# Optimization experiments

Measured on AMD Instinct MI355X. Metric: run time of the kernel, lower is better.

Reference implementation:

```python
import jax, jax.numpy as jnp
import numpy as np

EPS = 1e-5


def hetero_layernorm(x, node_type, gamma, beta):
    # LayerNorm over feature dim with per-node-type affine params.
    mu = jnp.mean(x, axis=-1, keepdims=True)
    var = jnp.mean(jnp.square(x - mu), axis=-1, keepdims=True)
    xn = (x - mu) * jax.lax.rsqrt(var + EPS)
    return xn * gamma[node_type] + beta[node_type]


def rgcn_conv(y, edge_src, edge_dst, edge_type, W_rel, W_root):
    # Transform per relation first (R small), then gather per-edge message.
    n = y.shape[0]
    h = jnp.einsum('nd,rde->rne', y, W_rel)          # [R, N, d]
    msg = h[edge_type, edge_src]                     # [E, d] gather
    agg = jax.ops.segment_sum(msg, edge_dst, num_segments=n)  # [N, d]
    return agg + y @ W_root


def hetero_mlp(y, node_type, W_mlp, b_mlp):
    # Per-node-type linear: compute for all T types, then select.
    n = y.shape[0]
    h = jnp.einsum('nd,tde->tne', y, W_mlp) + b_mlp[:, None, :]  # [T, N, d]
    return h[node_type, jnp.arange(n)]


def setup_inputs() -> dict:
    key = jax.random.key(0)
    ks = jax.random.split(key, 8)
    N, E, D, T, R = 50000, 800000, 128, 4, 8
    x = jax.random.normal(ks[0], (N, D), dtype=jnp.float32)
    edge_src = jax.random.randint(ks[1], (E,), 0, N, dtype=jnp.int32)
    edge_dst = jax.random.randint(ks[2], (E,), 0, N, dtype=jnp.int32)
    node_type = jax.random.randint(ks[3], (N,), 0, T, dtype=jnp.int32)
    edge_type = jax.random.randint(ks[4], (E,), 0, R, dtype=jnp.int32)
    # Scale weights ~ 1/sqrt(fan_in) for stable magnitudes.
    s = 1.0 / np.sqrt(D)
    W_rel = jax.random.normal(ks[5], (R, D, D), dtype=jnp.float32) * s
    W_root = jax.random.normal(ks[6], (D, D), dtype=jnp.float32) * s
    W_mlp = jax.random.normal(ks[7], (T, D, D), dtype=jnp.float32) * s
    return {
        'x': x, 'edge_src': edge_src, 'edge_dst': edge_dst,
        'node_type': node_type, 'edge_type': edge_type,
        'conv_gamma': jnp.ones((T, D), jnp.float32),
        'conv_beta': jnp.zeros((T, D), jnp.float32),
        'W_rel': W_rel, 'W_root': W_root,
        'mlp_gamma': jnp.ones((T, D), jnp.float32),
        'mlp_beta': jnp.zeros((T, D), jnp.float32),
        'W_mlp': W_mlp, 'b_mlp': jnp.zeros((T, D), jnp.float32),
    }


def reference(x, edge_src, edge_dst, node_type, edge_type,
              conv_gamma, conv_beta, W_rel, W_root,
              mlp_gamma, mlp_beta, W_mlp, b_mlp):
    # Norm -> Act -> (Dropout p=0, eval) -> Conv -> Residual
    y = hetero_layernorm(x, node_type, conv_gamma, conv_beta)
    y = jax.nn.relu(y)
    x = x + rgcn_conv(y, edge_src, edge_dst, edge_type, W_rel, W_root)
    # Norm -> Act -> (Dropout p=0, eval) -> MLP -> Residual
    y = hetero_layernorm(x, node_type, mlp_gamma, mlp_beta)
    y = jax.nn.relu(y)
    x = x + hetero_mlp(y, node_type, W_mlp, b_mlp)
    return x
```

## Files before the change

kernel.cpp:

```cpp
#include <hip/hip_runtime.h>
#include <hip/hip_bf16.h>

#define D 128
#define EPS 1e-5f
#define CHK 8192
#define P2CAP 6144

typedef __attribute__((ext_vector_type(8))) short short8;
typedef __attribute__((ext_vector_type(4))) float float4v;

#define AS1 __attribute__((address_space(1)))
#define AS3 __attribute__((address_space(3)))

__device__ inline ushort f2bf(float f) {
    __hip_bfloat16 b = __float2bfloat16(f);
    return *reinterpret_cast<ushort*>(&b);
}
__device__ inline float bf_lo(uint u) { return __uint_as_float(u << 16); }
__device__ inline float bf_hi(uint u) { return __uint_as_float(u & 0xffff0000u); }

__global__ void k_ln1cvt(const float* __restrict__ x, const int* __restrict__ ntp,
                         const float* __restrict__ gamma, const float* __restrict__ beta,
                         ushort* __restrict__ y,
                         const float* __restrict__ Wrel, const float* __restrict__ Wroot,
                         const float* __restrict__ Wmlp, ushort* __restrict__ Wt, int N) {
    __shared__ ushort t[128][136];
    if (blockIdx.x < 13) {
        int m = blockIdx.x;
        const float* src = (m == 0) ? Wroot
                         : (m <= 8) ? Wrel + (size_t)(m - 1) * D * D
                                    : Wmlp + (size_t)(m - 9) * D * D;
        for (int i = threadIdx.x; i < D * D; i += 256) {
            int k = i >> 7, n = i & 127;
            t[n][k] = f2bf(src[i]);
        }
        __syncthreads();
        ushort* dst = Wt + (size_t)m * D * D;
        for (int i = threadIdx.x; i < D * D; i += 256) {
            int frag = i >> 9;
            int lane = (i >> 3) & 63;
            int j = i & 7;
            int nt = frag >> 2, ks = frag & 3;
            int n = nt * 16 + (lane & 15);
            int k = ks * 32 + (lane >> 4) * 8 + j;
            dst[i] = t[n][k];
        }
        return;
    }
    int n = (blockIdx.x - 13) * 4 + (threadIdx.x >> 6);
    if (n >= N) return;
    int l = threadIdx.x & 63;
    float2 v = *(const float2*)(x + (size_t)n * D + 2 * l);
    float s = v.x + v.y, s2 = v.x * v.x + v.y * v.y;
    #pragma unroll
    for (int o = 32; o; o >>= 1) { s += __shfl_xor(s, o, 64); s2 += __shfl_xor(s2, o, 64); }
    float mu = s * (1.0f / D);
    float var = s2 * (1.0f / D) - mu * mu;
    float inv = rsqrtf(var + EPS);
    int tt = ntp[n];
    float2 g = *(const float2*)(gamma + tt * D + 2 * l);
    float2 b = *(const float2*)(beta + tt * D + 2 * l);
    float a0 = fmaxf((v.x - mu) * inv * g.x + b.x, 0.0f);
    float a1 = fmaxf((v.y - mu) * inv * g.y + b.y, 0.0f);
    ((uint*)(y + (size_t)n * D))[l] = ((uint)f2bf(a1) << 16) | f2bf(a0);
}

__global__ void k_c1(const int* __restrict__ edst, int* __restrict__ hist, int E, int B) {
    __shared__ int cnt[256];
    int c = blockIdx.x, tid = threadIdx.x;
    cnt[tid] = 0;
    __syncthreads();
    #pragma unroll 4
    for (int k = 0; k < CHK / 256; ++k) {
        int e = c * CHK + k * 256 + tid;
        if (e < E) atomicAdd(&cnt[edst[e] >> 8], 1);
    }
    __syncthreads();
    if (tid < B) hist[c * B + tid] = cnt[tid];
}
__global__ void k_c2(const int* __restrict__ hist, int* __restrict__ chunkoff,
                     int* __restrict__ bucktot, int C, int B) {
    __shared__ int v[128];
    int b = blockIdx.x, t = threadIdx.x;
    v[t] = (t < C) ? hist[t * B + b] : 0;
    __syncthreads();
    if (t == 0) {
        int s = 0;
        for (int c = 0; c < C; ++c) { int x = v[c]; v[c] = s; s += x; }
        bucktot[b] = s;
    }
    __syncthreads();
    if (t < C) chunkoff[t * B + b] = v[t];
}
__global__ void k_p1s(const int* __restrict__ edst, const int* __restrict__ esrc,
                      const int* __restrict__ etyp, const int* __restrict__ bucktot,
                      const int* __restrict__ chunkoff, uint* __restrict__ edata,
                      int E, int B) {
    __shared__ int ps[256];
    __shared__ int base[256];
    __shared__ int cnt[256];
    int c = blockIdx.x, tid = threadIdx.x;
    int bt = (tid < B) ? bucktot[tid] : 0;
    ps[tid] = bt;
    __syncthreads();
    for (int o = 1; o < 256; o <<= 1) {
        int v = (tid >= o) ? ps[tid - o] : 0;
        __syncthreads();
        ps[tid] += v;
        __syncthreads();
    }
    base[tid] = (ps[tid] - bt) + ((tid < B) ? chunkoff[c * B + tid] : 0);
    cnt[tid] = 0;
    __syncthreads();
    #pragma unroll 4
    for (int k = 0; k < CHK / 256; ++k) {
        int e = c * CHK + k * 256 + tid;
        if (e < E) {
            int d = edst[e];
            int b = d >> 8;
            int r = atomicAdd(&cnt[b], 1);
            edata[base[b] + r] =
                ((uint)esrc[e] << 12) | ((uint)(d & 255) << 4) | (uint)etyp[e];
        }
    }
}
__global__ void k_p2(const uint* __restrict__ edata, const int* __restrict__ bucktot,
                     uint* __restrict__ epack, int* __restrict__ offs,
                     int N, int E, int B) {
    __shared__ int ps[256];
    __shared__ uint ed[P2CAP];
    __shared__ int cnt[256], off[256], cur[256];
    int b = blockIdx.x, tid = threadIdx.x;
    int bt = (tid < B) ? bucktot[tid] : 0;
    ps[tid] = bt;
    __syncthreads();
    for (int o = 1; o < 256; o <<= 1) {
        int v = (tid >= o) ? ps[tid - o] : 0;
        __syncthreads();
        ps[tid] += v;
        __syncthreads();
    }
    int j0 = ps[b] - ((b < B) ? bucktot[b] : 0);
    int count = ps[b] - j0;
    if (count > P2CAP) count = P2CAP;
    for (int i = tid; i < count; i += 256) ed[i] = edata[j0 + i];
    cnt[tid] = 0;
    __syncthreads();
    for (int i = tid; i < count; i += 256) atomicAdd(&cnt[(ed[i] >> 4) & 255], 1);
    __syncthreads();
    if (tid == 0) {
        int s = 0;
        for (int i = 0; i < 256; ++i) { off[i] = s; cur[i] = s; s += cnt[i]; }
    }
    __syncthreads();
    for (int i = tid; i < count; i += 256) {
        uint v = ed[i];
        int dl = (v >> 4) & 255;
        int r = atomicAdd(&cur[dl], 1);
        epack[j0 + r] = ((v & 15u) << 28) | (v >> 12);
    }
    int v = b * 256 + tid;
    if (v < N) offs[v] = j0 + off[tid];
    if (b == 0 && tid == 0) offs[N] = E;
}

__global__ void k_zagg(const ushort* __restrict__ ybuf, const int* __restrict__ offs,
                       const uint* __restrict__ epack, ushort* __restrict__ zbuf, int N) {
    int wave = threadIdx.x >> 6;
    int l = threadIdx.x & 63;
    int v = blockIdx.x * 4 + wave;
    if (v >= N) return;
    float2 a0 = {0.f,0.f}, a1 = {0.f,0.f}, a2 = {0.f,0.f}, a3 = {0.f,0.f};
    float2 a4 = {0.f,0.f}, a5 = {0.f,0.f}, a6 = {0.f,0.f}, a7 = {0.f,0.f};
    const uint* yb = (const uint*)ybuf;
    int j = offs[v], e1 = offs[v + 1];

#define ZACC(P, U) do {                                                   \
        float lo = bf_lo(U), hi = bf_hi(U);                               \
        switch ((P) >> 28) {                                              \
            case 0: a0.x += lo; a0.y += hi; break;                        \
            case 1: a1.x += lo; a1.y += hi; break;                        \
            case 2: a2.x += lo; a2.y += hi; break;                        \
            case 3: a3.x += lo; a3.y += hi; break;                        \
            case 4: a4.x += lo; a4.y += hi; break;                        \
            case 5: a5.x += lo; a5.y += hi; break;                        \
            case 6: a6.x += lo; a6.y += hi; break;                        \
            default: a7.x += lo; a7.y += hi; break;                       \
        }                                                                 \
    } while (0)

    while (j < e1) {
        int chunk = min(64, e1 - j);
        uint pl = (j + l < e1) ? epack[j + l] : 0;
        int i = 0;
        for (; i + 3 < chunk; i += 4) {
            uint p0 = __shfl(pl, i, 64);
            uint p1 = __shfl(pl, i + 1, 64);
            uint p2 = __shfl(pl, i + 2, 64);
            uint p3 = __shfl(pl, i + 3, 64);
            uint u0 = yb[(size_t)(p0 & 0x0FFFFFFFu) * 64 + l];
            uint u1 = yb[(size_t)(p1 & 0x0FFFFFFFu) * 64 + l];
            uint u2 = yb[(size_t)(p2 & 0x0FFFFFFFu) * 64 + l];
            uint u3 = yb[(size_t)(p3 & 0x0FFFFFFFu) * 64 + l];
            ZACC(p0, u0); ZACC(p1, u1); ZACC(p2, u2); ZACC(p3, u3);
        }
        for (; i < chunk; ++i) {
            uint p = __shfl(pl, i, 64);
            uint u = yb[(size_t)(p & 0x0FFFFFFFu) * 64 + l];
            ZACC(p, u);
        }
        j += chunk;
    }
#undef ZACC
    uint* zrow = (uint*)(zbuf + (size_t)v * 1024);
    zrow[0 * 64 + l] = ((uint)f2bf(a0.y) << 16) | f2bf(a0.x);
    zrow[1 * 64 + l] = ((uint)f2bf(a1.y) << 16) | f2bf(a1.x);
    zrow[2 * 64 + l] = ((uint)f2bf(a2.y) << 16) | f2bf(a2.x);
    zrow[3 * 64 + l] = ((uint)f2bf(a3.y) << 16) | f2bf(a3.x);
    zrow[4 * 64 + l] = ((uint)f2bf(a4.y) << 16) | f2bf(a4.x);
    zrow[5 * 64 + l] = ((uint)f2bf(a5.y) << 16) | f2bf(a5.x);
    zrow[6 * 64 + l] = ((uint)f2bf(a6.y) << 16) | f2bf(a6.x);
    zrow[7 * 64 + l] = ((uint)f2bf(a7.y) << 16) | f2bf(a7.x);
}

__device__ __forceinline__ void gl_lds16(const void* g, void* l) {
    __builtin_amdgcn_global_load_lds((const AS1 void*)g, (AS3 void*)l, 16, 0, 0);
}
__device__ __forceinline__ void stage_half(const ushort* __restrict__ Wt, int q,
                                           ushort* bsm0, int wave, int lane) {
    const char* g = (const char*)Wt + (size_t)q * 16384 + lane * 16;
    char* l = (char*)bsm0 + (q & 1) * 16384;
    #pragma unroll
    for (int i = 0; i < 4; ++i) {
        int c = i * 4 + wave;
        gl_lds16(g + c * 1024, l + c * 1024);
    }
}
__device__ __forceinline__ void stage_mlp_slice(const ushort* __restrict__ Wt, int nt,
                                                ushort* bsm0, int wave, int lane) {
    const char* g = (const char*)Wt + (size_t)(9 + wave) * 32768 + nt * 4096 + lane * 16;
    char* l = (char*)bsm0 + (nt & 1) * 16384 + wave * 4096;
    #pragma unroll
    for (int i = 0; i < 4; ++i)
        gl_lds16(g + i * 1024, l + i * 1024);
}
__device__ __forceinline__ void aloadG(short8 (&d)[4], const ushort* p, int off, int ao) {
    #pragma unroll
    for (int ks = 0; ks < 4; ++ks)
        d[ks] = *(const short8*)(p + off + ks * 32 + ao);
}
__device__ __forceinline__ void convHalf(float4v (&acc)[8], const short8 (&a)[4],
                                         const ushort* bsm_h, int h, int lane) {
    #pragma unroll
    for (int nt4 = 0; nt4 < 4; ++nt4) {
        #pragma unroll
        for (int ks = 0; ks < 4; ++ks) {
            short8 b = *(const short8*)(bsm_h + (((nt4 * 4 + ks) * 64 + lane) << 3));
            acc[h * 4 + nt4] = __builtin_amdgcn_mfma_f32_16x16x32_bf16(
                a[ks], b, acc[h * 4 + nt4], 0, 0, 0);
        }
    }
}

__launch_bounds__(256, 4)
__global__ void k_gm(const ushort* __restrict__ ybuf, const ushort* __restrict__ zbuf,
                     const ushort* __restrict__ Wt, const float* __restrict__ x,
                     const int* __restrict__ ntp,
                     const float* __restrict__ gamma, const float* __restrict__ beta,
                     const float* __restrict__ bmlp, float* __restrict__ out, int N) {
    __shared__ ushort bsm[2][8192];
    ushort* bsm0 = &bsm[0][0];
    int tid = threadIdx.x;
    int wave = tid >> 6, lane = tid & 63;
    int quad = lane >> 4, l15 = lane & 15;
    int ao = quad * 8;
    int base = blockIdx.x * 64 + wave * 16;

    const ushort* yrow = ybuf + (size_t)min(base + l15, N - 1) * 128;
    const ushort* zrow = zbuf + (size_t)min(base + l15, N - 1) * 1024;

    float4v acc[8];
    #pragma unroll
    for (int nt = 0; nt < 8; ++nt) acc[nt] = (float4v){0.f, 0.f, 0.f, 0.f};

    short8 aC[4], aN[4];
    stage_half(Wt, 0, bsm0, wave, lane);
    aloadG(aC, yrow, 0, ao);
    __syncthreads();

    #pragma unroll
    for (int m = 0; m < 9; ++m) {
        short8 (&cur)[4] = (m & 1) ? aN : aC;
        short8 (&nxt)[4] = (m & 1) ? aC : aN;
        stage_half(Wt, 2 * m + 1, bsm0, wave, lane);
        if (m < 8) aloadG(nxt, zrow, m * 128, ao);
        convHalf(acc, cur, bsm0, 0, lane);
        __syncthreads();
        if (m < 8) stage_half(Wt, 2 * m + 2, bsm0, wave, lane);
        else       stage_mlp_slice(Wt, 0, bsm0, wave, lane);
        convHalf(acc, cur, bsm0 + 8192, 1, lane);
        __syncthreads();
    }

    ushort* yov = bsm0 + 8192 + wave * 2048;
    int ty[4];
    {
        float s[4] = {0.f, 0.f, 0.f, 0.f}, s2[4] = {0.f, 0.f, 0.f, 0.f};
        #pragma unroll
        for (int nt = 0; nt < 8; ++nt) {
            int col = nt * 16 + l15;
            #pragma unroll
            for (int r = 0; r < 4; ++r) {
                int row = base + quad * 4 + r;
                float xv = (row < N) ? x[(size_t)row * D + col] : 0.f;
                float t = acc[nt][r] + xv;
                acc[nt][r] = t;
                s[r] += t; s2[r] += t * t;
            }
        }
        #pragma unroll
        for (int r = 0; r < 4; ++r) {
            #pragma unroll
            for (int o = 1; o < 16; o <<= 1) {
                s[r]  += __shfl_xor(s[r],  o, 64);
                s2[r] += __shfl_xor(s2[r], o, 64);
            }
        }
        #pragma unroll
        for (int r = 0; r < 4; ++r) {
            int rc = min(base + quad * 4 + r, N - 1);
            ty[r] = ntp[rc];
            float mu  = s[r] * (1.0f / D);
            float var = s2[r] * (1.0f / D) - mu * mu;
            float inv = rsqrtf(var + EPS);
            int lrow = quad * 4 + r;
            #pragma unroll
            for (int nt = 0; nt < 8; ++nt) {
                int col = nt * 16 + l15;
                float yn = fmaxf((acc[nt][r] - mu) * inv * gamma[ty[r] * D + col]
                                 + beta[ty[r] * D + col], 0.f);
                yov[lrow * 128 + col] = f2bf(yn);
            }
        }
    }
    short8 a2[4];
    {
        const ushort* myrow = yov + l15 * 128;
        #pragma unroll
        for (int ks = 0; ks < 4; ++ks) a2[ks] = *(const short8*)(myrow + ks * 32 + ao);
    }
    __syncthreads();

    #pragma unroll
    for (int nt = 0; nt < 8; ++nt) {
        if (nt < 7) stage_mlp_slice(Wt, nt + 1, bsm0, wave, lane);
        const ushort* bh = bsm0 + (nt & 1) * 8192;
        float4v c0 = {0.f,0.f,0.f,0.f}, c1 = {0.f,0.f,0.f,0.f};
        float4v c2 = {0.f,0.f,0.f,0.f}, c3 = {0.f,0.f,0.f,0.f};
        #pragma unroll
        for (int ks = 0; ks < 4; ++ks) {
            int fo = (ks * 64 + lane) << 3;
            short8 b0 = *(const short8*)(bh + 0 * 2048 + fo);
            short8 b1 = *(const short8*)(bh + 1 * 2048 + fo);
            short8 b2 = *(const short8*)(bh + 2 * 2048 + fo);
            short8 b3 = *(const short8*)(bh + 3 * 2048 + fo);
            c0 = __builtin_amdgcn_mfma_f32_16x16x32_bf16(a2[ks], b0, c0, 0, 0, 0);
            c1 = __builtin_amdgcn_mfma_f32_16x16x32_bf16(a2[ks], b1, c1, 0, 0, 0);
            c2 = __builtin_amdgcn_mfma_f32_16x16x32_bf16(a2[ks], b2, c2, 0, 0, 0);
            c3 = __builtin_amdgcn_mfma_f32_16x16x32_bf16(a2[ks], b3, c3, 0, 0, 0);
        }
        int col = nt * 16 + l15;
        #pragma unroll
        for (int r = 0; r < 4; ++r) {
            int row = base + quad * 4 + r;
            if (row < N) {
                int t = ty[r];
                float v = (t == 0) ? c0[r] : (t == 1) ? c1[r] : (t == 2) ? c2[r] : c3[r];
                out[(size_t)row * D + col] = acc[nt][r] + v + bmlp[t * D + col];
            }
        }
        if (nt < 7) __syncthreads();
    }
}

extern "C" void kernel_launch(void* const* d_in, const int* in_sizes, int n_in,
                              void* d_out, int out_size, void* d_ws, size_t ws_size,
                              hipStream_t stream) {
    const float* x          = (const float*)d_in[0];
    const int*   esrc       = (const int*)d_in[1];
    const int*   edst       = (const int*)d_in[2];
    const int*   ntyp       = (const int*)d_in[3];
    const int*   etyp       = (const int*)d_in[4];
    const float* conv_gamma = (const float*)d_in[5];
    const float* conv_beta  = (const float*)d_in[6];
    const float* W_rel      = (const float*)d_in[7];
    const float* W_root     = (const float*)d_in[8];
    const float* mlp_gamma  = (const float*)d_in[9];
    const float* mlp_beta   = (const float*)d_in[10];
    const float* W_mlp      = (const float*)d_in[11];
    const float* b_mlp      = (const float*)d_in[12];
    float* out = (float*)d_out;

    int N = in_sizes[0] / D;
    int E = in_sizes[1];
    int C = (E + CHK - 1) / CHK;
    int B = (N + 255) / 256;

    char* p = (char*)d_ws;
    auto take = [&p](size_t bytes) { char* q = p; p += (bytes + 255) & ~(size_t)255; return q; };
    ushort* ybuf    = (ushort*)take((size_t)N * D * 2);
    ushort* zbuf    = (ushort*)take((size_t)N * 1024 * 2);
    ushort* Wt      = (ushort*)take((size_t)13 * D * D * 2);
    uint*   edata   = (uint*)take((size_t)E * 4);
    uint*   epack   = (uint*)take((size_t)E * 4);
    int*    offs    = (int*)take((size_t)(N + 1) * 4);
    int*    hist    = (int*)take((size_t)C * B * 4);
    int*    chunkoff= (int*)take((size_t)C * B * 4);
    int*    bucktot = (int*)take((size_t)B * 4);

    k_ln1cvt<<<13 + (N + 3) / 4, 256, 0, stream>>>(x, ntyp, conv_gamma, conv_beta,
                                                   ybuf, W_rel, W_root, W_mlp, Wt, N);

    k_c1<<<C, 256, 0, stream>>>(edst, hist, E, B);
    k_c2<<<B, 128, 0, stream>>>(hist, chunkoff, bucktot, C, B);
    k_p1s<<<C, 256, 0, stream>>>(edst, esrc, etyp, bucktot, chunkoff, edata, E, B);
    k_p2<<<B, 256, 0, stream>>>(edata, bucktot, epack, offs, N, E, B);

    k_zagg<<<(N + 3) / 4, 256, 0, stream>>>(ybuf, offs, epack, zbuf, N);

    k_gm<<<(N + 63) / 64, 256, 0, stream>>>(ybuf, zbuf, Wt, x, ntyp,
                                            mlp_gamma, mlp_beta, b_mlp, out, N);
}
```

Measured before the change: 275.5 us.

## Replace two-level bucket sort CSR build with global atomic histogram, scan, scatter

Replaces the four-kernel chunked bucket sort (histogram, chunk offsets, partial scatter, per-bucket local sort) with a simpler CSR build. Per-destination degree counting is folded into the layernorm kernel through global atomics, followed by a single-block scan and an atomic-slot scatter of packed (type, src) edges. This cuts kernel launches and the intermediate edata pass. In exchange it relies on heavy global atomic contention, a serial single-block scan over N+1 entries, and non-deterministic edge order within each destination, which can change float summation order.

After: 338.5 us. 1.23x slower.

```diff
diff --git a/kernel.cpp b/kernel.cpp
--- a/kernel.cpp
+++ b/kernel.cpp
@@ -3,8 +3,6 @@
 
 #define D 128
 #define EPS 1e-5f
-#define CHK 8192
-#define P2CAP 6144
 
 typedef __attribute__((ext_vector_type(8))) short short8;
 typedef __attribute__((ext_vector_type(4))) float float4v;
@@ -23,7 +21,13 @@
                          const float* __restrict__ gamma, const float* __restrict__ beta,
                          ushort* __restrict__ y,
                          const float* __restrict__ Wrel, const float* __restrict__ Wroot,
-                         const float* __restrict__ Wmlp, ushort* __restrict__ Wt, int N) {
+                         const float* __restrict__ Wmlp, ushort* __restrict__ Wt,
+                         const int* __restrict__ edst, int* __restrict__ offs,
+                         int N, int E) {
+    {
+        int e = blockIdx.x * 64 + threadIdx.x;
+        if (threadIdx.x < 64 && e < E) atomicAdd(&offs[edst[e] + 1], 1);
+    }
     __shared__ ushort t[128][136];
     if (blockIdx.x < 13) {
         int m = blockIdx.x;
@@ -65,103 +69,55 @@
     ((uint*)(y + (size_t)n * D))[l] = ((uint)f2bf(a1) << 16) | f2bf(a0);
 }
 
-__global__ void k_c1(const int* __restrict__ edst, int* __restrict__ hist, int E, int B) {
-    __shared__ int cnt[256];
-    int c = blockIdx.x, tid = threadIdx.x;
-    cnt[tid] = 0;
+__global__ void k_scan(int* __restrict__ offs, int* __restrict__ cur, int N) {
+    __shared__ int wsum[16];
+    __shared__ int carryS;
+    int tid = threadIdx.x, lane = tid & 63, w = tid >> 6;
+    int N1 = N + 1;
+    if (tid == 0) carryS = 0;
     __syncthreads();
-    #pragma unroll 4
-    for (int k = 0; k < CHK / 256; ++k) {
-        int e = c * CHK + k * 256 + tid;
-        if (e < E) atomicAdd(&cnt[edst[e] >> 8], 1);
-    }
-    __syncthreads();
-    if (tid < B) hist[c * B + tid] = cnt[tid];
-}
-__global__ void k_c2(const int* __restrict__ hist, int* __restrict__ chunkoff,
-                     int* __restrict__ bucktot, int C, int B) {
-    __shared__ int v[128];
-    int b = blockIdx.x, t = threadIdx.x;
-    v[t] = (t < C) ? hist[t * B + b] : 0;
-    __syncthreads();
-    if (t == 0) {
-        int s = 0;
-        for (int c = 0; c < C; ++c) { int x = v[c]; v[c] = s; s += x; }
-        bucktot[b] = s;
-    }
-    __syncthreads();
-    if (t < C) chunkoff[t * B + b] = v[t];
-}
-__global__ void k_p1s(const int* __restrict__ edst, const int* __restrict__ esrc,
-                      const int* __restrict__ etyp, const int* __restrict__ bucktot,
-                      const int* __restrict__ chunkoff, uint* __restrict__ edata,
-                      int E, int B) {
-    __shared__ int ps[256];
-    __shared__ int base[256];
-    __shared__ int cnt[256];
-    int c = blockIdx.x, tid = threadIdx.x;
-    int bt = (tid < B) ? bucktot[tid] : 0;
-    ps[tid] = bt;
-    __syncthreads();
-    for (int o = 1; o < 256; o <<= 1) {
-        int v = (tid >= o) ? ps[tid - o] : 0;
-        __syncthreads();
-        ps[tid] += v;
-        __syncthreads();
-    }
-    base[tid] = (ps[tid] - bt) + ((tid < B) ? chunkoff[c * B + tid] : 0);
-    cnt[tid] = 0;
-    __syncthreads();
-    #pragma unroll 4
-    for (int k = 0; k < CHK / 256; ++k) {
-        int e = c * CHK + k * 256 + tid;
-        if (e < E) {
-            int d = edst[e];
-            int b = d >> 8;
-            int r = atomicAdd(&cnt[b], 1);
-            edata[base[b] + r] =
-                ((uint)esrc[e] << 12) | ((uint)(d & 255) << 4) | (uint)etyp[e];
-        }
-    }
-}
-__global__ void k_p2(const uint* __restrict__ edata, const int* __restrict__ bucktot,
-                     uint* __restrict__ epack, int* __restrict__ offs,
-                     int N, int E, int B) {
-    __shared__ int ps[256];
-    __shared__ uint ed[P2CAP];
-    __shared__ int cnt[256], off[256], cur[256];
-    int b = blockIdx.x, tid = threadIdx.x;
-    int bt = (tid < B) ? bucktot[tid] : 0;
-    ps[tid] = bt;
-    __syncthreads();
-    for (int o = 1; o < 256; o <<= 1) {
-        int v = (tid >= o) ? ps[tid - o] : 0;
-        __syncthreads();
-        ps[tid] += v;
-        __syncthreads();
-    }
-    int j0 = ps[b] - ((b < B) ? bucktot[b] : 0);
-    int count = ps[b] - j0;
-    if (count > P2CAP) count = P2CAP;
-    for (int i = tid; i < count; i += 256) ed[i] = edata[j0 + i];
-    cnt[tid] = 0;
-    __syncthreads();
-    for (int i = tid; i < count; i += 256) atomicAdd(&cnt[(ed[i] >> 4) & 255], 1);
-    __syncthreads();
-    if (tid == 0) {
-        int s = 0;
-        for (int i = 0; i < 256; ++i) { off[i] = s; cur[i] = s; s += cnt[i]; }
-    }
-    __syncthreads();
-    for (int i = tid; i < count; i += 256) {
-        uint v = ed[i];
-        int dl = (v >> 4) & 255;
-        int r = atomicAdd(&cur[dl], 1);
-        epack[j0 + r] = ((v & 15u) << 28) | (v >> 12);
-    }
-    int v = b * 256 + tid;
-    if (v < N) offs[v] = j0 + off[tid];
-    if (b == 0 && tid == 0) offs[N] = E;
+    for (int base = 0; base < N1; base += 1024) {
+        int i = base + tid;
+        int v = (i < N1) ? offs[i] : 0;
+        int s = v;
+        #pragma unroll
+        for (int o = 1; o < 64; o <<= 1) {
+            int t = __shfl_up(s, o, 64);
+            if (lane >= o) s += t;
+        }
+        if (lane == 63) wsum[w] = s;
+        __syncthreads();
+        if (w == 0) {
+            int t = (lane < 16) ? wsum[lane] : 0;
+            #pragma unroll
+            for (int o = 1; o < 16; o <<= 1) {
+                int u = __shfl_up(t, o, 64);
+                if (lane >= o) t += u;
+            }
+            if (lane < 16) wsum[lane] = t;
+        }
+        __syncthreads();
+        int carry = carryS;
+        int res = s + carry + (w ? wsum[w - 1] : 0);
+        if (i < N1) {
+            offs[i] = res;
+            if (i < N) cur[i] = res;
+        }
+        __syncthreads();
+        if (tid == 0) carryS = carry + wsum[15];
+        __syncthreads();
+    }
+}
+
+__global__ void k_scatter(const int* __restrict__ esrc, const int* __restrict__ edst,
+                          const int* __restrict__ etyp, int* __restrict__ cur,
+                          uint* __restrict__ epack, int E) {
+    int e = blockIdx.x * 256 + threadIdx.x;
+    if (e < E) {
+        int d = edst[e];
+        int slot = atomicAdd(&cur[d], 1);
+        epack[slot] = ((uint)etyp[e] << 28) | (uint)esrc[e];
+    }
 }
 
 __global__ void k_zagg(const ushort* __restrict__ ybuf, const int* __restrict__ offs,
@@ -403,28 +359,26 @@
 
     int N = in_sizes[0] / D;
     int E = in_sizes[1];
-    int C = (E + CHK - 1) / CHK;
-    int B = (N + 255) / 256;
 
     char* p = (char*)d_ws;
     auto take = [&p](size_t bytes) { char* q = p; p += (bytes + 255) & ~(size_t)255; return q; };
     ushort* ybuf    = (ushort*)take((size_t)N * D * 2);
     ushort* zbuf    = (ushort*)take((size_t)N * 1024 * 2);
     ushort* Wt      = (ushort*)take((size_t)13 * D * D * 2);
-    uint*   edata   = (uint*)take((size_t)E * 4);
     uint*   epack   = (uint*)take((size_t)E * 4);
     int*    offs    = (int*)take((size_t)(N + 1) * 4);
-    int*    hist    = (int*)take((size_t)C * B * 4);
-    int*    chunkoff= (int*)take((size_t)C * B * 4);
-    int*    bucktot = (int*)take((size_t)B * 4);
-
-    k_ln1cvt<<<13 + (N + 3) / 4, 256, 0, stream>>>(x, ntyp, conv_gamma, conv_beta,
-                                                   ybuf, W_rel, W_root, W_mlp, Wt, N);
-
-    k_c1<<<C, 256, 0, stream>>>(edst, hist, E, B);
-    k_c2<<<B, 128, 0, stream>>>(hist, chunkoff, bucktot, C, B);
-    k_p1s<<<C, 256, 0, stream>>>(edst, esrc, etyp, bucktot, chunkoff, edata, E, B);
-    k_p2<<<B, 256, 0, stream>>>(edata, bucktot, epack, offs, N, E, B);
+    int*    cur     = (int*)take((size_t)N * 4);
+
+    hipMemsetAsync(offs, 0, (size_t)(N + 1) * 4, stream);
+
+    int gridLn = 13 + (N + 3) / 4;
+    int gridE64 = (E + 63) / 64;
+    int grid1 = gridLn > gridE64 ? gridLn : gridE64;
+    k_ln1cvt<<<grid1, 256, 0, stream>>>(x, ntyp, conv_gamma, conv_beta, ybuf,
+                                        W_rel, W_root, W_mlp, Wt, edst, offs, N, E);
+
+    k_scan<<<1, 1024, 0, stream>>>(offs, cur, N);
+    k_scatter<<<(E + 255) / 256, 256, 0, stream>>>(esrc, edst, etyp, cur, epack, E);
 
     k_zagg<<<(N + 3) / 4, 256, 0, stream>>>(ybuf, offs, epack, zbuf, N);
 
```
